# Optimization experiments

Measured on AMD Instinct MI355X. Metric: run time of the kernel, lower is better.

The kernel has to match this reference:

```python
import jax, jax.numpy as jnp
import numpy as np
from jax import lax

NEG = -1e30  # log-space 'zero' that stays finite for stable grads


def _logadd3(a, b, c):
    m = jnp.maximum(jnp.maximum(a, b), c)
    return m + jnp.log(jnp.exp(a - m) + jnp.exp(b - m) + jnp.exp(c - m))


def _logadd2(a, b):
    m = jnp.maximum(a, b)
    return m + jnp.log(jnp.exp(a - m) + jnp.exp(b - m))


def setup_inputs() -> dict:
    key = jax.random.key(0)
    k1, k2, k3 = jax.random.split(key, 3)
    B, T, V, L = 64, 2000, 512, 200
    logits = jax.random.normal(k1, (B, T, V), dtype=jnp.float32)
    # keep input lengths well above 2*L+1 so all paths are feasible
    input_lengths = (T - jax.random.randint(k2, (B,), 0, 256)).astype(jnp.int32)
    targets = jax.random.randint(k3, (B, L), 0, V, dtype=jnp.int32)  # 0 == pad == blank
    return {"logits": logits, "input_lengths": input_lengths, "targets": targets}


def ctc_loss_sum(logits, input_lengths, targets):
    B, T, V = logits.shape
    L = targets.shape[1]
    S = 2 * L + 1

    lp = jax.nn.log_softmax(logits, axis=-1)  # [B,T,V]

    # compact nonzero targets per row (masked_select equivalent, fixed shape)
    mask = targets != 0
    tlen = mask.sum(-1)  # [B] target_lengths
    pos = jnp.where(mask, jnp.cumsum(mask, axis=1) - 1, L)
    compact = jnp.zeros_like(targets).at[jnp.arange(B)[:, None], pos].set(targets, mode="drop")

    # extended label sequence: blank, y1, blank, y2, ..., blank  -> [B,S]
    s_idx = jnp.arange(S)
    lab_idx = jnp.clip((s_idx - 1) // 2, 0, L - 1)
    ext = jnp.where(s_idx % 2 == 1, compact[:, lab_idx], 0)  # [B,S]

    # skip transition s-2 -> s allowed iff label at s is non-blank and differs from s-2
    ext_m2 = jnp.pad(ext, ((0, 0), (2, 0)))[:, :S]
    skip_ok = (ext != 0) & (ext != ext_m2) & (s_idx >= 2)  # [B,S]

    lpT = jnp.transpose(lp, (1, 0, 2))  # [T,B,V], scan over time

    # init: alpha_0[0]=lp(blank), alpha_0[1]=lp(y1)
    lp0_ext = jnp.take_along_axis(lpT[0], ext[:, :2], axis=1)  # [B,2]
    alpha0 = jnp.full((B, S), NEG, dtype=lp.dtype).at[:, :2].set(lp0_ext)

    def step(alpha, inp):
        lp_t, t = inp
        a1 = jnp.pad(alpha, ((0, 0), (1, 0)), constant_values=NEG)[:, :S]
        a2 = jnp.pad(alpha, ((0, 0), (2, 0)), constant_values=NEG)[:, :S]
        a2 = jnp.where(skip_ok, a2, NEG)
        lp_e = jnp.take_along_axis(lp_t, ext, axis=1)  # [B,S]
        new = _logadd3(alpha, a1, a2) + lp_e
        active = (t < input_lengths)[:, None]
        return jnp.where(active, new, alpha), None

    alphaT, _ = lax.scan(step, alpha0, (lpT[1:], jnp.arange(1, T)))

    # read out at final blank (2*tlen) and final label (2*tlen-1)
    e1 = (2 * tlen)[:, None]
    e2 = (2 * tlen - 1)
    a1 = jnp.take_along_axis(alphaT, e1, axis=1)[:, 0]
    a2 = jnp.where(e2 >= 0,
                   jnp.take_along_axis(alphaT, jnp.clip(e2, 0)[:, None], axis=1)[:, 0],
                   NEG)
    ll = _logadd2(a1, a2)  # [B] log p(targets | logits)
    return -jnp.sum(ll)


def reference(logits, input_lengths, targets):
    return ctc_loss_sum(logits, input_lengths, targets)
```

## Files before the change

### kernel.cpp

```cpp
#include <hip/hip_runtime.h>

#define B_ 64
#define T_ 2000
#define V_ 512
#define L_ 200
#define NJB 63
#define NCH 250


typedef _Float16 half4 __attribute__((ext_vector_type(4)));
typedef unsigned long long ull;
typedef ull u64x2 __attribute__((ext_vector_type(2)));
union H4U { unsigned long long u; half4 h; };

__device__ __forceinline__ float dpp_shr1_f(float x) {
  return __int_as_float(__builtin_amdgcn_update_dpp(0, __float_as_int(x), 0x138, 0xf, 0xf, true));
}
__device__ __forceinline__ int dpp_shr1_i(int x) {
  return __builtin_amdgcn_update_dpp(0, x, 0x138, 0xf, 0xf, true);
}
__device__ __forceinline__ float dpp_shl1_f(float x) {
  return __int_as_float(__builtin_amdgcn_update_dpp(0, __float_as_int(x), 0x130, 0xf, 0xf, true));
}
__device__ __forceinline__ int dpp_shl1_i(int x) {
  return __builtin_amdgcn_update_dpp(0, x, 0x130, 0xf, 0xf, true);
}
#define DPPADD(v, ctrl, rmask)                                                              \
  v += __int_as_float(__builtin_amdgcn_update_dpp(0, __float_as_int(v), ctrl, rmask, 0xf, true));

#define COMPACT(BB)                                                          \
  int base = 0;                                                              \
  {                                                                          \
    cmp[lane] = 0; cmp[64 + lane] = 0; cmp[128 + lane] = 0; cmp[192 + lane] = 0; \
    _Pragma("unroll") for (int cc = 0; cc < 4; ++cc) {                       \
      const int l = cc * 64 + lane;                                          \
      const int v = (l < L_) ? targets[(BB) * L_ + l] : 0;                   \
      const unsigned long long mk = __ballot(v != 0);                        \
      const int pos = base + __popcll(mk & ((1ull << lane) - 1ull));         \
      if (v != 0) cmp[pos] = v;                                              \
      base += __popcll(mk);                                                  \
    }                                                                        \
    asm volatile("s_waitcnt lgkmcnt(0)" ::: "memory");                       \
  }

__global__ __launch_bounds__(256, 4) void kprob(const float* __restrict__ logits,
                                                const int* __restrict__ lens,
                                                const int* __restrict__ targets,
                                                u64x2* __restrict__ cull2,
                                                float* __restrict__ bl) {
  const int tid = threadIdx.x;
  const int wid = tid >> 6;
  const int lane = tid & 63;
  __shared__ int cmp[256];
  __shared__ __align__(16) float scr[4][2][512];

  const int g = blockIdx.x;
  const int b = g & 63;
  const int jb = g >> 6;
  const int len = lens[b];
  const int nch = (len + 7) >> 3;
  if (wid == 0) { COMPACT(b); }
  __syncthreads();
  const int c = jb * 4 + wid;
  if (c >= nch) return;

  const int4 c4 = *(const int4*)(&cmp[4 * lane]);
  const int l0 = 4 * lane;
  const bool v0 = l0 + 0 < L_, v1 = l0 + 1 < L_, v2 = l0 + 2 < L_, v3 = l0 + 3 < L_;

  const float* rowp = logits + (size_t)b * (T_ * V_) + (size_t)c * (8 * V_);
  float4 X[16];
#pragma unroll
  for (int r = 0; r < 8; ++r) {
    X[2 * r] = *(const float4*)(rowp + r * V_ + 4 * lane);
    X[2 * r + 1] = *(const float4*)(rowp + r * V_ + 256 + 4 * lane);
  }
  u64x2* outp = cull2 + ((size_t)(b * NCH + c) * 4) * 64 + lane;
  unsigned long long pe = 0;
  float blb[8];
#pragma unroll
  for (int r = 0; r < 8; ++r) {
    const float4 xe = X[2 * r], xo = X[2 * r + 1];
    const float e0 = __expf(xe.x), e1 = __expf(xe.y), e2 = __expf(xe.z), e3 = __expf(xe.w);
    const float e4 = __expf(xo.x), e5 = __expf(xo.y), e6 = __expf(xo.z), e7 = __expf(xo.w);
    float s = ((e0 + e1) + (e2 + e3)) + ((e4 + e5) + (e6 + e7));
    DPPADD(s, 0x111, 0xf); DPPADD(s, 0x112, 0xf); DPPADD(s, 0x114, 0xf);
    DPPADD(s, 0x118, 0xf); DPPADD(s, 0x142, 0xa); DPPADD(s, 0x143, 0xc);
    const float sum = __int_as_float(__builtin_amdgcn_readlane(__float_as_int(s), 63));
    const float inv = 32.0f / sum;
    float* sc = &scr[wid][r & 1][0];
    *(float4*)(sc + 4 * lane) = make_float4(e0, e1, e2, e3);
    *(float4*)(sc + 256 + 4 * lane) = make_float4(e4, e5, e6, e7);
    asm volatile("s_waitcnt lgkmcnt(0)" ::: "memory");
    H4U p;
    p.h.x = (_Float16)(v0 ? sc[c4.x] * inv : 0.0f);
    p.h.y = (_Float16)(v1 ? sc[c4.y] * inv : 0.0f);
    p.h.z = (_Float16)(v2 ? sc[c4.z] * inv : 0.0f);
    p.h.w = (_Float16)(v3 ? sc[c4.w] * inv : 0.0f);
    if (r & 1) {
      u64x2 w; w.x = pe; w.y = p.u;
      outp[(r >> 1) * 64] = w;
    } else {
      pe = p.u;
    }
    blb[r] = e0 * inv;
  }
  if (lane == 0) {
    float4* bp = (float4*)(bl + b * 2048 + c * 8);
    bp[0] = make_float4(blb[0], blb[1], blb[2], blb[3]);
    bp[1] = make_float4(blb[4], blb[5], blb[6], blb[7]);
  }
}

__global__ __launch_bounds__(64) void krec(const int* __restrict__ lens,
                                           const int* __restrict__ targets,
                                           const u64x2* __restrict__ cull2,
                                           const float* __restrict__ bl,
                                           float* __restrict__ AF, int* __restrict__ EF,
                                           float* __restrict__ DD, int* __restrict__ EB) {
  const int lane = threadIdx.x;
  __shared__ int cmp[256];
  const int b = blockIdx.x >> 1;
  const int dirb = blockIdx.x & 1;
  const int len = lens[b];
  const int rem = len & 7;
  const int nch = (len + 7) >> 3;
  const int Cf = nch >> 1;
  const int Ntot = dirb ? (nch - Cf) : Cf;
  const int c0v = dirb ? (nch - 1) : 0;
  const int dstep = dirb ? -1 : 1;
#define CHK(J) (c0v + dstep * (J))

  COMPACT(b);
  const int tl = base;
  const int4 c4 = *(const int4*)(&cmp[4 * lane]);

  const int cm1 = __shfl_up(c4.w, 1);
  const float m0 = (lane > 0 && c4.x != 0 && c4.x != cm1) ? 1.0f : 0.0f;
  const float m1 = (c4.y != 0 && c4.y != c4.x) ? 1.0f : 0.0f;
  const float m2 = (c4.z != 0 && c4.z != c4.y) ? 1.0f : 0.0f;
  const float m3 = (c4.w != 0 && c4.w != c4.z) ? 1.0f : 0.0f;
  const float m0n = dpp_shl1_f(m0);

  float a0 = 0.f, a1 = 0.f, a2 = 0.f, a3 = 0.f, a4 = 0.f, a5 = 0.f, a6 = 0.f, a7 = 0.f;
  int E = 0;
  float fac = 1.0f;
  if (!dirb) {
    if (lane == 0) a0 = 1.0f;
  } else {
    const int st = 2 * tl;
    if (lane == (st >> 3)) {
      const int e = st & 7;
      a0 = (e == 0) ? 1.0f : 0.0f; a1 = (e == 1) ? 1.0f : 0.0f;
      a2 = (e == 2) ? 1.0f : 0.0f; a3 = (e == 3) ? 1.0f : 0.0f;
      a4 = (e == 4) ? 1.0f : 0.0f; a5 = (e == 5) ? 1.0f : 0.0f;
      a6 = (e == 6) ? 1.0f : 0.0f; a7 = (e == 7) ? 1.0f : 0.0f;
    }
  }

  u64x2 Qa0, Qb0, Qc0, Qd0, Qa1, Qb1, Qc1, Qd1, Qa2, Qb2, Qc2, Qd2;
  u64x2 Qa3, Qb3, Qc3, Qd3, Qa4, Qb4, Qc4, Qd4, Qa5, Qb5, Qc5, Qd5;
  float4 BLa0, BLb0, BLa1, BLb1, BLa2, BLb2, BLa3, BLb3, BLa4, BLb4, BLa5, BLb5;

#define LOADC(S, CIDX)                                                       \
  {                                                                          \
    const int c_ = (CIDX);                                                   \
    const u64x2* pp_ = cull2 + ((size_t)(b * NCH + c_) * 4) * 64 + lane;     \
    Qa##S = pp_[0]; Qb##S = pp_[64]; Qc##S = pp_[128]; Qd##S = pp_[192];     \
    const float* bf_ = bl + b * 2048 + c_ * 8;                               \
    BLa##S = *(const float4*)(bf_);                                          \
    BLb##S = *(const float4*)(bf_ + 4);                                      \
  }

#define STEP8F(S)                                                            \
  {                                                                          \
    const float blv_[8] = {BLa##S.x, BLa##S.y, BLa##S.z, BLa##S.w,           \
                           BLb##S.x, BLb##S.y, BLb##S.z, BLb##S.w};          \
    const unsigned long long qu_[8] = {Qa##S.x, Qa##S.y, Qb##S.x, Qb##S.y,   \
                                       Qc##S.x, Qc##S.y, Qd##S.x, Qd##S.y};  \
    _Pragma("unroll") for (int u = 0; u < 8; ++u) {                          \
      H4U q_; q_.u = qu_[u];                                                 \
      const float qx = (float)q_.h.x, qy = (float)q_.h.y;                    \
      const float qz = (float)q_.h.z, qw = (float)q_.h.w;                    \
      const float pbv = blv_[u];                                             \
      const float s1 = dpp_shr1_f(a7) * fac;                 \
      float n0 = (a0 + s1) * pbv;                                            \
      float n1 = fmaf(m0, s1, a0 + a1) * qx;                                 \
      float n2 = (a2 + a1) * pbv;                                            \
      float n3 = fmaf(m1, a1, a2 + a3) * qy;                                 \
      float n4 = (a4 + a3) * pbv;                                            \
      float n5 = fmaf(m2, a3, a4 + a5) * qz;                                 \
      float n6 = (a6 + a5) * pbv;                                            \
      float n7 = fmaf(m3, a5, a6 + a7) * qw;                                 \
      a0 = n0; a1 = n1; a2 = n2; a3 = n3;                                    \
      a4 = n4; a5 = n5; a6 = n6; a7 = n7;                                    \
    }                                                                        \
  }

#define STEP8B(S, UHI)                                                       \
  {                                                                          \
    const float blv_[8] = {BLa##S.x, BLa##S.y, BLa##S.z, BLa##S.w,           \
                           BLb##S.x, BLb##S.y, BLb##S.z, BLb##S.w};          \
    const unsigned long long qu_[8] = {Qa##S.x, Qa##S.y, Qb##S.x, Qb##S.y,   \
                                       Qc##S.x, Qc##S.y, Qd##S.x, Qd##S.y};  \
    _Pragma("unroll") for (int u = 7; u >= 0; --u) {                         \
      if (u <= (UHI)) {                                                      \
        H4U q_; q_.u = qu_[u];                                               \
        const float qx = (float)q_.h.x, qy = (float)q_.h.y;                  \
        const float qz = (float)q_.h.z, qw = (float)q_.h.w;                  \
        const float pbv = blv_[u];                                           \
        const float sa = dpp_shl1_f(a0) * fac;              \
        const float sb = dpp_shl1_f(a1) * fac;                               \
        float n0 = (a0 + a1) * pbv;                                          \
        float n1 = fmaf(m1, a3, a1 + a2) * qx;                               \
        float n2 = (a2 + a3) * pbv;                                          \
        float n3 = fmaf(m2, a5, a3 + a4) * qy;                               \
        float n4 = (a4 + a5) * pbv;                                          \
        float n5 = fmaf(m3, a7, a5 + a6) * qz;                               \
        float n6 = (a6 + a7) * pbv;                                          \
        float n7 = fmaf(m0n, sb, a7 + sa) * qw;                              \
        a0 = n0; a1 = n1; a2 = n2; a3 = n3;                                  \
        a4 = n4; a5 = n5; a6 = n6; a7 = n7;                                  \
      }                                                                      \
    }                                                                        \
  }

#define RENORM_COMMON                                                        \
    const float mx = fmaxf(fmaxf(fmaxf(a0, a1), fmaxf(a2, a3)),              \
                           fmaxf(fmaxf(a4, a5), fmaxf(a6, a7)));             \
    const bool dead = (mx == 0.0f);                                          \
    int e_ = (int)((__float_as_uint(mx) >> 23) & 0xff) - 127;                \
    if (dead) e_ = 0;                                                        \
    const float sc_ = __int_as_float((unsigned)(127 - e_) << 23);            \
    a0 *= sc_; a1 *= sc_; a2 *= sc_; a3 *= sc_;                              \
    a4 *= sc_; a5 *= sc_; a6 *= sc_; a7 *= sc_;                              \
    const int En_ = E + e_;

#define RENORMF                                                              \
  {                                                                          \
    RENORM_COMMON                                                            \
    const int EnP_ = dpp_shr1_i(En_);                                        \
    E = dead ? EnP_ : En_;                                                   \
    const int Ep_ = dpp_shr1_i(E);                                           \
    const int d_ = Ep_ - E;                                                  \
    int dc_ = d_ < -126 ? -126 : (d_ > 126 ? 126 : d_);                      \
    fac = (d_ < -126) ? 0.0f : __int_as_float((unsigned)(dc_ + 127) << 23);  \
  }

#define RENORMB                                                              \
  {                                                                          \
    RENORM_COMMON                                                            \
    const int EnP_ = dpp_shl1_i(En_);                                        \
    E = dead ? EnP_ : En_;                                                   \
    const int Ep_ = dpp_shl1_i(E);                                           \
    const int d_ = Ep_ - E;                                                  \
    int dc_ = d_ < -126 ? -126 : (d_ > 126 ? 126 : d_);                      \
    fac = (d_ < -126) ? 0.0f : __int_as_float((unsigned)(dc_ + 127) << 23);  \
  }

  LOADC(0, CHK(0)); LOADC(1, CHK(1)); LOADC(2, CHK(2));
  LOADC(3, CHK(3)); LOADC(4, CHK(4)); LOADC(5, CHK(5));
  int i = 0;

  if (!dirb) {
    STEP8F(0); LOADC(0, CHK(6));  RENORMF;
    STEP8F(1); LOADC(1, CHK(7));  RENORMF;
    STEP8F(2); LOADC(2, CHK(8));  RENORMF;
    STEP8F(3); LOADC(3, CHK(9));  RENORMF;
    STEP8F(4); LOADC(4, CHK(10)); RENORMF;
    STEP8F(5); LOADC(5, CHK(11)); RENORMF;
    i = 6;
    while (i + 12 <= Ntot) {
      STEP8F(0); LOADC(0, CHK(i + 6));  RENORMF;
      STEP8F(1); LOADC(1, CHK(i + 7));  RENORMF;
      STEP8F(2); LOADC(2, CHK(i + 8));  RENORMF;
      STEP8F(3); LOADC(3, CHK(i + 9));  RENORMF;
      STEP8F(4); LOADC(4, CHK(i + 10)); RENORMF;
      STEP8F(5); LOADC(5, CHK(i + 11)); RENORMF;
      i += 6;
    }
    const int r2 = Ntot - i;
    for (int k = 0; k < r2; ++k) {
      const int nx = i + k + 6;
      const bool pf = nx < Ntot;
      switch (k % 6) {
        case 0: STEP8F(0); RENORMF; if (pf) LOADC(0, CHK(nx)); break;
        case 1: STEP8F(1); RENORMF; if (pf) LOADC(1, CHK(nx)); break;
        case 2: STEP8F(2); RENORMF; if (pf) LOADC(2, CHK(nx)); break;
        case 3: STEP8F(3); RENORMF; if (pf) LOADC(3, CHK(nx)); break;
        case 4: STEP8F(4); RENORMF; if (pf) LOADC(4, CHK(nx)); break;
        default: STEP8F(5); RENORMF; if (pf) LOADC(5, CHK(nx)); break;
      }
    }
    *(float4*)(AF + b * 512 + lane * 8) = make_float4(a0, a1, a2, a3);
    *(float4*)(AF + b * 512 + lane * 8 + 4) = make_float4(a4, a5, a6, a7);
    EF[b * 64 + lane] = E;
  } else {
    const int uh0 = rem ? (rem - 1) : 7;
    STEP8B(0, uh0); LOADC(0, CHK(6));  RENORMB;
    STEP8B(1, 7);   LOADC(1, CHK(7));  RENORMB;
    STEP8B(2, 7);   LOADC(2, CHK(8));  RENORMB;
    STEP8B(3, 7);   LOADC(3, CHK(9));  RENORMB;
    STEP8B(4, 7);   LOADC(4, CHK(10)); RENORMB;
    STEP8B(5, 7);   LOADC(5, CHK(11)); RENORMB;
    i = 6;
    while (i + 12 <= Ntot) {
      STEP8B(0, 7); LOADC(0, CHK(i + 6));  RENORMB;
      STEP8B(1, 7); LOADC(1, CHK(i + 7));  RENORMB;
      STEP8B(2, 7); LOADC(2, CHK(i + 8));  RENORMB;
      STEP8B(3, 7); LOADC(3, CHK(i + 9));  RENORMB;
      STEP8B(4, 7); LOADC(4, CHK(i + 10)); RENORMB;
      STEP8B(5, 7); LOADC(5, CHK(i + 11)); RENORMB;
      i += 6;
    }
    const int r2 = Ntot - i;
    for (int k = 0; k < r2; ++k) {
      const int nx = i + k + 6;
      const bool pf = nx < Ntot;
      switch (k % 6) {
        case 0: STEP8B(0, 7); RENORMB; if (pf) LOADC(0, CHK(nx)); break;
        case 1: STEP8B(1, 7); RENORMB; if (pf) LOADC(1, CHK(nx)); break;
        case 2: STEP8B(2, 7); RENORMB; if (pf) LOADC(2, CHK(nx)); break;
        case 3: STEP8B(3, 7); RENORMB; if (pf) LOADC(3, CHK(nx)); break;
        case 4: STEP8B(4, 7); RENORMB; if (pf) LOADC(4, CHK(nx)); break;
        default: STEP8B(5, 7); RENORMB; if (pf) LOADC(5, CHK(nx)); break;
      }
    }
    const float sa = dpp_shl1_f(a0) * fac;
    const float sb = dpp_shl1_f(a1) * fac;
    const float d0 = a0 + a1;
    const float d1 = fmaf(m1, a3, a1 + a2);
    const float d2 = a2 + a3;
    const float d3 = fmaf(m2, a5, a3 + a4);
    const float d4 = a4 + a5;
    const float d5 = fmaf(m3, a7, a5 + a6);
    const float d6 = a6 + a7;
    const float d7 = fmaf(m0n, sb, a7 + sa);
    *(float4*)(DD + b * 512 + lane * 8) = make_float4(d0, d1, d2, d3);
    *(float4*)(DD + b * 512 + lane * 8 + 4) = make_float4(d4, d5, d6, d7);
    EB[b * 64 + lane] = E;
  }
#undef LOADC
#undef STEP8F
#undef STEP8B
#undef RENORM_COMMON
#undef RENORMF
#undef RENORMB
#undef CHK
}

__global__ __launch_bounds__(512) void kcomb(const int* __restrict__ lens,
                                             const float* __restrict__ AF,
                                             const int* __restrict__ EF,
                                             const float* __restrict__ DD,
                                             const int* __restrict__ EB,
                                             float* __restrict__ out) {
  const int wid = threadIdx.x >> 6;
  const int lane = threadIdx.x & 63;
  __shared__ float part[8];
  float acc = 0.0f;
#pragma unroll
  for (int q = 0; q < 8; ++q) {
    const int b = wid * 8 + q;
    const float4 f0 = *(const float4*)(AF + b * 512 + lane * 8);
    const float4 f1 = *(const float4*)(AF + b * 512 + lane * 8 + 4);
    const float4 g0 = *(const float4*)(DD + b * 512 + lane * 8);
    const float4 g1 = *(const float4*)(DD + b * 512 + lane * 8 + 4);
    const float dot = ((f0.x * g0.x + f0.y * g0.y) + (f0.z * g0.z + f0.w * g0.w)) +
                      ((f1.x * g1.x + f1.y * g1.y) + (f1.z * g1.z + f1.w * g1.w));
    const int Es = EF[b * 64 + lane] + EB[b * 64 + lane];
    const bool z = (dot == 0.0f);
    int Ek = z ? (-(1 << 28)) : Es;
#pragma unroll
    for (int off = 32; off; off >>= 1) {
      const int o = __shfl_xor(Ek, off);
      Ek = o > Ek ? o : Ek;
    }
    float v = z ? 0.0f : ldexpf(dot, Es - Ek);
#pragma unroll
    for (int off = 32; off; off >>= 1) v += __shfl_xor(v, off);
    const float ll = __logf(v) + (float)Ek * 0.69314718056f - (float)lens[b] * 3.46573590280f;
    acc -= ll;
  }
  if (lane == 0) part[wid] = acc;
  __syncthreads();
  if (threadIdx.x == 0) {
    float s = ((part[0] + part[1]) + (part[2] + part[3])) +
              ((part[4] + part[5]) + (part[6] + part[7]));
    out[0] = s;
  }
}

extern "C" void kernel_launch(void* const* d_in, const int* in_sizes, int n_in,
                              void* d_out, int out_size, void* d_ws, size_t ws_size,
                              hipStream_t stream) {
  const float* logits = (const float*)d_in[0];
  const int* input_lengths = (const int*)d_in[1];
  const int* targets = (const int*)d_in[2];
  float* out = (float*)d_out;
  u64x2* cull2 = (u64x2*)d_ws;
  float* bl = (float*)((char*)d_ws + 65536000);
  float* AF = (float*)((char*)d_ws + 66125824);
  int* EF = (int*)((char*)d_ws + 66256896);
  float* DD = (float*)((char*)d_ws + 66273280);
  int* EB = (int*)((char*)d_ws + 66404352);
  (void)in_sizes; (void)n_in; (void)out_size; (void)ws_size;

  kprob<<<B_ * NJB, 256, 0, stream>>>(logits, input_lengths, targets, cull2, bl);
  krec<<<2 * B_, 64, 0, stream>>>(input_lengths, targets, cull2, bl, AF, EF, DD, EB);
  kcomb<<<1, 512, 0, stream>>>(input_lengths, AF, EF, DD, EB, out);
}
```

Before: 435.5 us.

## Process four chunks per wave in kprob with double-buffered register prefetch

The softmax/gather kernel now launches a quarter as many blocks, and each wave handles four time chunks spaced 64 apart. Loads for the next chunk are issued into a second register buffer while the current chunk is processed, and the LDS scratch is widened to 8 rows so all exps are written before a single wait. This is meant to hide global load latency and cut per-block launch and compaction overhead. In exchange, register and LDS use per block roughly doubles, so occupancy drops (launch bounds lowered from 4 to 2 blocks per CU), and chunk C is loaded without a bounds check against nch.

```diff
diff --git a/kernel.cpp b/kernel.cpp
--- a/kernel.cpp
+++ b/kernel.cpp
@@ -4,7 +4,7 @@
 #define T_ 2000
 #define V_ 512
 #define L_ 200
-#define NJB 63
+#define NJB 16
 #define NCH 250
 
 
@@ -43,7 +43,7 @@
     asm volatile("s_waitcnt lgkmcnt(0)" ::: "memory");                       \
   }
 
-__global__ __launch_bounds__(256, 4) void kprob(const float* __restrict__ logits,
+__global__ __launch_bounds__(256, 2) void kprob(const float* __restrict__ logits,
                                                 const int* __restrict__ lens,
                                                 const int* __restrict__ targets,
                                                 u64x2* __restrict__ cull2,
@@ -52,7 +52,7 @@
   const int wid = tid >> 6;
   const int lane = tid & 63;
   __shared__ int cmp[256];
-  __shared__ __align__(16) float scr[4][2][512];
+  __shared__ __align__(16) float scr[4][8][512];
 
   const int g = blockIdx.x;
   const int b = g & 63;
@@ -61,55 +61,77 @@
   const int nch = (len + 7) >> 3;
   if (wid == 0) { COMPACT(b); }
   __syncthreads();
-  const int c = jb * 4 + wid;
-  if (c >= nch) return;
+  const int slot = jb * 4 + wid;
 
   const int4 c4 = *(const int4*)(&cmp[4 * lane]);
   const int l0 = 4 * lane;
   const bool v0 = l0 + 0 < L_, v1 = l0 + 1 < L_, v2 = l0 + 2 < L_, v3 = l0 + 3 < L_;
-
-  const float* rowp = logits + (size_t)b * (T_ * V_) + (size_t)c * (8 * V_);
-  float4 X[16];
-#pragma unroll
-  for (int r = 0; r < 8; ++r) {
-    X[2 * r] = *(const float4*)(rowp + r * V_ + 4 * lane);
-    X[2 * r + 1] = *(const float4*)(rowp + r * V_ + 256 + 4 * lane);
-  }
-  u64x2* outp = cull2 + ((size_t)(b * NCH + c) * 4) * 64 + lane;
-  unsigned long long pe = 0;
-  float blb[8];
-#pragma unroll
-  for (int r = 0; r < 8; ++r) {
-    const float4 xe = X[2 * r], xo = X[2 * r + 1];
-    const float e0 = __expf(xe.x), e1 = __expf(xe.y), e2 = __expf(xe.z), e3 = __expf(xe.w);
-    const float e4 = __expf(xo.x), e5 = __expf(xo.y), e6 = __expf(xo.z), e7 = __expf(xo.w);
-    float s = ((e0 + e1) + (e2 + e3)) + ((e4 + e5) + (e6 + e7));
-    DPPADD(s, 0x111, 0xf); DPPADD(s, 0x112, 0xf); DPPADD(s, 0x114, 0xf);
-    DPPADD(s, 0x118, 0xf); DPPADD(s, 0x142, 0xa); DPPADD(s, 0x143, 0xc);
-    const float sum = __int_as_float(__builtin_amdgcn_readlane(__float_as_int(s), 63));
-    const float inv = 32.0f / sum;
-    float* sc = &scr[wid][r & 1][0];
-    *(float4*)(sc + 4 * lane) = make_float4(e0, e1, e2, e3);
-    *(float4*)(sc + 256 + 4 * lane) = make_float4(e4, e5, e6, e7);
-    asm volatile("s_waitcnt lgkmcnt(0)" ::: "memory");
-    H4U p;
-    p.h.x = (_Float16)(v0 ? sc[c4.x] * inv : 0.0f);
-    p.h.y = (_Float16)(v1 ? sc[c4.y] * inv : 0.0f);
-    p.h.z = (_Float16)(v2 ? sc[c4.z] * inv : 0.0f);
-    p.h.w = (_Float16)(v3 ? sc[c4.w] * inv : 0.0f);
-    if (r & 1) {
-      u64x2 w; w.x = pe; w.y = p.u;
-      outp[(r >> 1) * 64] = w;
-    } else {
-      pe = p.u;
-    }
-    blb[r] = e0 * inv;
-  }
-  if (lane == 0) {
-    float4* bp = (float4*)(bl + b * 2048 + c * 8);
-    bp[0] = make_float4(blb[0], blb[1], blb[2], blb[3]);
-    bp[1] = make_float4(blb[4], blb[5], blb[6], blb[7]);
-  }
+  const float* bbase = logits + (size_t)b * (T_ * V_);
+
+  float4 XA[16], XB[16];
+
+#define LOADX(BUF, C)                                                        \
+  {                                                                          \
+    const float* rp_ = bbase + (size_t)(C) * (8 * V_);                       \
+    _Pragma("unroll") for (int r = 0; r < 8; ++r) {                          \
+      X##BUF[2 * r] = *(const float4*)(rp_ + r * V_ + 4 * lane);             \
+      X##BUF[2 * r + 1] = *(const float4*)(rp_ + r * V_ + 256 + 4 * lane);   \
+    }                                                                        \
+  }
+
+#define PROC(BUF, C)                                                         \
+  {                                                                          \
+    float inv_[8], blb_[8];                                                  \
+    _Pragma("unroll") for (int r = 0; r < 8; ++r) {                          \
+      const float4 xe = X##BUF[2 * r], xo = X##BUF[2 * r + 1];               \
+      const float e0 = __expf(xe.x), e1 = __expf(xe.y);                      \
+      const float e2 = __expf(xe.z), e3 = __expf(xe.w);                      \
+      const float e4 = __expf(xo.x), e5 = __expf(xo.y);                      \
+      const float e6 = __expf(xo.z), e7 = __expf(xo.w);                      \
+      float s = ((e0 + e1) + (e2 + e3)) + ((e4 + e5) + (e6 + e7));           \
+      DPPADD(s, 0x111, 0xf); DPPADD(s, 0x112, 0xf); DPPADD(s, 0x114, 0xf);   \
+      DPPADD(s, 0x118, 0xf); DPPADD(s, 0x142, 0xa); DPPADD(s, 0x143, 0xc);   \
+      const float sum = __int_as_float(__builtin_amdgcn_readlane(__float_as_int(s), 63)); \
+      const float iv = 32.0f / sum;       \
+      inv_[r] = iv;                                                          \
+      blb_[r] = e0 * iv;               \
+      float* sc_ = &scr[wid][r][0];                                          \
+      *(float4*)(sc_ + 4 * lane) = make_float4(e0, e1, e2, e3);              \
+      *(float4*)(sc_ + 256 + 4 * lane) = make_float4(e4, e5, e6, e7);        \
+    }                                                                        \
+    asm volatile("s_waitcnt lgkmcnt(0)" ::: "memory");   \
+    u64x2* outp_ = cull2 + ((size_t)(b * NCH + (C)) * 4) * 64 + lane;        \
+    unsigned long long pe_ = 0;                                              \
+    _Pragma("unroll") for (int r = 0; r < 8; ++r) {                          \
+      const float* sc_ = &scr[wid][r][0];                                    \
+      const float iv = inv_[r];                                              \
+      H4U p;                                                                 \
+      p.h.x = (_Float16)(v0 ? sc_[c4.x] * iv : 0.0f);                        \
+      p.h.y = (_Float16)(v1 ? sc_[c4.y] * iv : 0.0f);                        \
+      p.h.z = (_Float16)(v2 ? sc_[c4.z] * iv : 0.0f);                        \
+      p.h.w = (_Float16)(v3 ? sc_[c4.w] * iv : 0.0f);                        \
+      if (r & 1) { u64x2 w_; w_.x = pe_; w_.y = p.u; outp_[(r >> 1) * 64] = w_; } \
+      else pe_ = p.u;                                                        \
+    }                                                                        \
+    if (lane == 0) {                                                         \
+      float4* bp_ = (float4*)(bl + b * 2048 + (C) * 8);                      \
+      bp_[0] = make_float4(blb_[0], blb_[1], blb_[2], blb_[3]);              \
+      bp_[1] = make_float4(blb_[4], blb_[5], blb_[6], blb_[7]);              \
+    }                                                                        \
+  }
+
+  const int cA = slot, cB = slot + 64, cC = slot + 128, cD = slot + 192;
+  const bool hasD = cD < nch;
+  LOADX(A, cA);
+  LOADX(B, cB);
+  PROC(A, cA);
+  LOADX(A, cC);
+  PROC(B, cB);
+  if (hasD) LOADX(B, cD);
+  PROC(A, cC);
+  if (hasD) PROC(B, cD);
+#undef LOADX
+#undef PROC
 }
 
 __global__ __launch_bounds__(64) void krec(const int* __restrict__ lens,
```

After: 439.8 us. Within noise of the previous version (+1.0%).
